# Kernel tuning notes

Measured on AMD Instinct MI355X. Metric: run time of the kernel, lower is better.

Reference implementation:

```python
import jax, jax.numpy as jnp
import numpy as np
import math

H = 16
D_MODEL = 1024
D_K = D_MODEL // H


def setup_inputs() -> dict:
    key = jax.random.key(0)
    ks = jax.random.split(key, 12)
    B, S = 4, 2048
    inp = {
        "query": jax.random.normal(ks[0], (B, S, D_MODEL), jnp.float32),
        "key": jax.random.normal(ks[1], (B, S, D_MODEL), jnp.float32),
        "value": jax.random.normal(ks[2], (B, S, D_MODEL), jnp.float32),
        # causal mask, broadcastable over heads: [B, 1, S, S]
        "mask": jnp.broadcast_to(jnp.tril(jnp.ones((S, S), bool)), (B, 1, S, S)),
    }
    sc = 1.0 / math.sqrt(D_MODEL)
    inp["Wq"] = jax.random.normal(ks[3], (D_MODEL, D_MODEL), jnp.float32) * sc
    inp["bq"] = jnp.zeros((D_MODEL,), jnp.float32)
    inp["Wk"] = jax.random.normal(ks[4], (D_MODEL, D_MODEL), jnp.float32) * sc
    inp["bk"] = jnp.zeros((D_MODEL,), jnp.float32)
    inp["Wv"] = jax.random.normal(ks[5], (D_MODEL, D_MODEL), jnp.float32) * sc
    inp["bv"] = jnp.zeros((D_MODEL,), jnp.float32)
    inp["Wo"] = jax.random.normal(ks[6], (D_MODEL, D_MODEL), jnp.float32) * sc
    inp["bo"] = jnp.zeros((D_MODEL,), jnp.float32)
    return inp


def reference(query, key, value, mask, Wq, bq, Wk, bk, Wv, bv, Wo, bo):
    B, S, D = query.shape
    # torch nn.Linear: y = x @ W.T + b; then view(B,-1,h,d_k).transpose(1,2)
    def proj(x, W, b):
        return (x @ W.T + b).reshape(B, -1, H, D_K).transpose(0, 2, 1, 3)  # [B,h,S,d_k]

    q = proj(query, Wq, bq)
    k = proj(key, Wk, bk)
    v = proj(value, Wv, bv)

    scores = jnp.einsum("bhqd,bhkd->bhqk", q, k) / math.sqrt(D_K)
    scores = jnp.where(mask, scores, jnp.finfo(scores.dtype).min)
    p_attn = jax.nn.softmax(scores, axis=-1)  # dropout: eval mode (identity)
    x = jnp.einsum("bhqk,bhkd->bhqd", p_attn, v)
    x = x.transpose(0, 2, 1, 3).reshape(B, -1, H * D_K)
    return x @ Wo.T + bo
```

## Files before the change

### kernel.cpp

```cpp
#include <hip/hip_runtime.h>
#include <hip/hip_bf16.h>

typedef unsigned short u16;
typedef unsigned int u32;
typedef __attribute__((ext_vector_type(8))) short short8;
typedef __attribute__((ext_vector_type(4))) short short4v;
typedef __attribute__((ext_vector_type(4))) float f32x4;
typedef __attribute__((ext_vector_type(4))) float float4_t;

#define DIM 1024
#define NH  16
#define DKK 64
#define SEQ 2048
#define NB  4
#define SM_SCALE 0.1803368801111244f

__device__ __forceinline__ u16 f2bf(float f) {
    __bf16 h = (__bf16)f;
    return __builtin_bit_cast(u16, h);
}

__device__ __forceinline__ f32x4 mfma_bf16(short8 a, short8 b, f32x4 c) {
    return __builtin_amdgcn_mfma_f32_16x16x32_bf16(a, b, c, 0, 0, 0);
}

__device__ __forceinline__ short8 pack8(float4_t a, float4_t b) {
    short8 v;
    v[0] = (short)f2bf(a[0]); v[1] = (short)f2bf(a[1]);
    v[2] = (short)f2bf(a[2]); v[3] = (short)f2bf(a[3]);
    v[4] = (short)f2bf(b[0]); v[5] = (short)f2bf(b[1]);
    v[6] = (short)f2bf(b[2]); v[7] = (short)f2bf(b[3]);
    return v;
}

typedef const __attribute__((address_space(1))) u32* gas1_t;
typedef __attribute__((address_space(3))) u32* las3_t;
__device__ __forceinline__ void g2l16(const void* g, void* l) {
    __builtin_amdgcn_global_load_lds((gas1_t)g, (las3_t)l, 16, 0, 0);
}

__device__ __forceinline__ float max16(const f32x4* s) {
    const float a = fmaxf(fmaxf(s[0][0], s[0][1]), fmaxf(s[0][2], s[0][3]));
    const float b = fmaxf(fmaxf(s[1][0], s[1][1]), fmaxf(s[1][2], s[1][3]));
    const float c = fmaxf(fmaxf(s[2][0], s[2][1]), fmaxf(s[2][2], s[2][3]));
    const float d = fmaxf(fmaxf(s[3][0], s[3][1]), fmaxf(s[3][2], s[3][3]));
    return fmaxf(fmaxf(a, b), fmaxf(c, d));
}

__global__ __launch_bounds__(256) void conv8(const float* __restrict__ src,
                                             u16* __restrict__ dst) {
    const int i = (blockIdx.x * 256 + threadIdx.x) * 8;
    const float4_t a = *(const float4_t*)(src + i);
    const float4_t b = *(const float4_t*)(src + i + 4);
    *(short8*)(dst + i) = pack8(a, b);
}

__global__ __launch_bounds__(256) void conv8w(const float* __restrict__ w0,
                                              const float* __restrict__ w1,
                                              const float* __restrict__ w2,
                                              const float* __restrict__ w3,
                                              u16* __restrict__ dst) {
    const int t = blockIdx.y;
    const float* s = t == 0 ? w0 : t == 1 ? w1 : t == 2 ? w2 : w3;
    const int i = (blockIdx.x * 256 + threadIdx.x) * 8;
    const float4_t a = *(const float4_t*)(s + i);
    const float4_t b = *(const float4_t*)(s + i + 4);
    *(short8*)(dst + (size_t)t * DIM * DIM + i) = pack8(a, b);
}

template<int MODE>
__global__ __launch_bounds__(256)
void gemmb(const u16* __restrict__ A, const u16* __restrict__ Bw,
           const float* __restrict__ bias, float scale,
           u16* __restrict__ Cbf, float* __restrict__ Cf)
{
    __shared__ __align__(16) u16 As[128][64];
    __shared__ __align__(16) u16 Bs[128][64];
    const int tid  = threadIdx.x;
    const int lane = tid & 63;
    const int w    = tid >> 6;
    const int wr   = w >> 1, wc = w & 1;
    const int m0   = blockIdx.y * 128;
    const int n0   = blockIdx.x * 128;
    const int lm   = lane & 15, lg = lane >> 4;
    const int srow   = lane >> 3;
    const int schunk = (lane & 7) ^ srow;

    f32x4 acc[4][4];
#pragma unroll
    for (int i = 0; i < 4; ++i)
#pragma unroll
        for (int j = 0; j < 4; ++j) acc[i][j] = (f32x4){0.f, 0.f, 0.f, 0.f};

    for (int k0 = 0; k0 < DIM; k0 += 64) {
        __syncthreads();
#pragma unroll
        for (int i = 0; i < 4; ++i) {
            g2l16(A  + (size_t)(m0 + w * 32 + i * 8 + srow) * DIM + k0 + schunk * 8,
                  &As[w * 32 + i * 8][0]);
            g2l16(Bw + (size_t)(n0 + w * 32 + i * 8 + srow) * DIM + k0 + schunk * 8,
                  &Bs[w * 32 + i * 8][0]);
        }
        __syncthreads();

        short8 af[2][4], bfr[2][4];
#pragma unroll
        for (int t = 0; t < 4; ++t)
#pragma unroll
            for (int kh = 0; kh < 2; ++kh) {
                const int c = (kh * 4 + lg) ^ (lm & 7);
                af[kh][t]  = *(const short8*)&As[wr * 64 + t * 16 + lm][c * 8];
                bfr[kh][t] = *(const short8*)&Bs[wc * 64 + t * 16 + lm][c * 8];
            }
#pragma unroll
        for (int mt = 0; mt < 4; ++mt)
#pragma unroll
            for (int nt = 0; nt < 4; ++nt) {
                acc[mt][nt] = mfma_bf16(af[0][mt], bfr[0][nt], acc[mt][nt]);
                acc[mt][nt] = mfma_bf16(af[1][mt], bfr[1][nt], acc[mt][nt]);
            }
    }

#pragma unroll
    for (int mt = 0; mt < 4; ++mt)
#pragma unroll
        for (int nt = 0; nt < 4; ++nt)
#pragma unroll
            for (int r = 0; r < 4; ++r) {
                const int m = m0 + wr * 64 + mt * 16 + lg * 4 + r;
                const int n = n0 + wc * 64 + nt * 16 + lm;
                if (MODE == 0) {
                    const float val = (acc[mt][nt][r] + bias[n]) * scale;
                    const int b = m >> 11, s = m & 2047;
                    const int h = n >> 6,  dk = n & 63;
                    Cbf[(((size_t)b * NH + h) * SEQ + s) * DKK + dk] = f2bf(val);
                } else if (MODE == 1) {
                    Cf[(size_t)m * DIM + n] = acc[mt][nt][r] + bias[n];
                } else {
                    const float val = acc[mt][nt][r] + bias[m];
                    const int h = m >> 6, dk = m & 63;
                    const int b = n >> 11, s = n & 2047;
                    Cbf[(((size_t)b * NH + h) * DKK + dk) * SEQ + s] = f2bf(val);
                }
            }
}

__global__ __launch_bounds__(256, 2)
void attn3(const u16* __restrict__ Q, const u16* __restrict__ K,
           const u16* __restrict__ Vt, u16* __restrict__ O)
{
    __shared__ __align__(16) u16 Ks[64][72];
    __shared__ __align__(16) u16 Vs[64][72];
    __shared__ __align__(16) u16 Ps[4][32][72];

    const int tid  = threadIdx.x;
    const int lane = tid & 63;
    const int w    = tid >> 6;
    const int lm   = lane & 15, lg = lane >> 4;
    const int Lr   = blockIdx.y * gridDim.x + blockIdx.x;
    const int work = (Lr & 7) * 128 + (Lr >> 3);
    const int pb   = work & 15;
    const int bh   = work >> 4;
    const int Abase = pb * 64;
    const int Bbase = SEQ - 64 - Abase;
    const int qA = Abase + 16 * w;
    const int qB = Bbase + 16 * w;
    const u16* Qp = Q  + (size_t)bh * SEQ * DKK;
    const u16* Kp = K  + (size_t)bh * SEQ * DKK;
    const u16* Vp = Vt + (size_t)bh * DKK * SEQ;

    short8 qa[2][2];
#pragma unroll
    for (int kh = 0; kh < 2; ++kh) {
        qa[0][kh] = *(const short8*)(Qp + (size_t)(qA + lm) * DKK + kh * 32 + lg * 8);
        qa[1][kh] = *(const short8*)(Qp + (size_t)(qB + lm) * DKK + kh * 32 + lg * 8);
    }

    float m_q[2] = {-INFINITY, -INFINITY};
    float l_q[2] = {0.f, 0.f};
    f32x4 o[2][4];
#pragma unroll
    for (int qt = 0; qt < 2; ++qt)
#pragma unroll
        for (int dt = 0; dt < 4; ++dt) o[qt][dt] = (f32x4){0.f, 0.f, 0.f, 0.f};

    const f32x4 zero = (f32x4){0.f, 0.f, 0.f, 0.f};
    const int srow = tid >> 3;
    const int soct = (tid & 7) * 8;
    const int kv_end = Bbase + 64;

    short8 rk0 = *(const short8*)(Kp + (size_t)srow * DKK + soct);
    short8 rk1 = *(const short8*)(Kp + (size_t)(srow + 32) * DKK + soct);
    short8 rv0 = *(const short8*)(Vp + (size_t)srow * SEQ + soct);
    short8 rv1 = *(const short8*)(Vp + (size_t)(srow + 32) * SEQ + soct);

    for (int kv0 = 0; kv0 < kv_end; kv0 += 64) {
        __syncthreads();
        *(short8*)&Ks[srow][soct]      = rk0;
        *(short8*)&Ks[srow + 32][soct] = rk1;
        *(short8*)&Vs[srow][soct]      = rv0;
        *(short8*)&Vs[srow + 32][soct] = rv1;
        const int nkv = kv0 + 64;
        if (nkv < kv_end) {
            rk0 = *(const short8*)(Kp + (size_t)(nkv + srow) * DKK + soct);
            rk1 = *(const short8*)(Kp + (size_t)(nkv + srow + 32) * DKK + soct);
            rv0 = *(const short8*)(Vp + (size_t)srow * SEQ + nkv + soct);
            rv1 = *(const short8*)(Vp + (size_t)(srow + 32) * SEQ + nkv + soct);
        }
        __syncthreads();

        const bool actA = kv0 < qA + 16;
        const bool msk[2] = { kv0 + 63 > qA, kv0 + 63 > qB };
        const int  qb[2]  = { qA, qB };

        f32x4 s[2][4];
#pragma unroll
        for (int kvt = 0; kvt < 4; ++kvt) {
            const short8 kb0 = *(const short8*)&Ks[kvt * 16 + lm][lg * 8];
            const short8 kb1 = *(const short8*)&Ks[kvt * 16 + lm][32 + lg * 8];
            s[1][kvt] = mfma_bf16(kb1, qa[1][1], mfma_bf16(kb0, qa[1][0], zero));
            if (actA)
                s[0][kvt] = mfma_bf16(kb1, qa[0][1], mfma_bf16(kb0, qa[0][0], zero));
        }

        float mx[2] = {-INFINITY, -INFINITY};
#pragma unroll
        for (int qt = 0; qt < 2; ++qt) {
            if (!qt && !actA) continue;
            if (msk[qt]) {
                const int q = qb[qt] + lm;
#pragma unroll
                for (int kvt = 0; kvt < 4; ++kvt)
#pragma unroll
                    for (int r = 0; r < 4; ++r) {
                        const int kv = kv0 + kvt * 16 + lg * 4 + r;
                        if (kv > q) s[qt][kvt][r] = -INFINITY;
                    }
            }
            float vmax = max16(s[qt]);
            vmax = fmaxf(vmax, __shfl_xor(vmax, 16));
            vmax = fmaxf(vmax, __shfl_xor(vmax, 32));
            mx[qt] = vmax;
        }

        const bool small = (!actA || mx[0] <= m_q[0] + 8.f) && (mx[1] <= m_q[1] + 8.f);
        if (__all(small)) {
#pragma unroll
            for (int qt = 0; qt < 2; ++qt) {
                if (!qt && !actA) continue;
                float part[4];
#pragma unroll
                for (int kvt = 0; kvt < 4; ++kvt) {
                    short4v pk;
                    f32x4 p;
#pragma unroll
                    for (int r = 0; r < 4; ++r) {
                        p[r] = __builtin_exp2f(s[qt][kvt][r] - m_q[qt]);
                        pk[r] = (short)f2bf(p[r]);
                    }
                    part[kvt] = (p[0] + p[1]) + (p[2] + p[3]);
                    *(short4v*)&Ps[w][qt * 16 + lm][kvt * 16 + lg * 4] = pk;
                }
                l_q[qt] += (part[0] + part[1]) + (part[2] + part[3]);
            }
        } else {
#pragma unroll
            for (int qt = 0; qt < 2; ++qt) {
                if (!qt && !actA) continue;
                const float mnew = fmaxf(m_q[qt], mx[qt]);
                const float alpha = __builtin_exp2f(m_q[qt] - mnew);
                m_q[qt] = mnew;
                float part[4];
#pragma unroll
                for (int kvt = 0; kvt < 4; ++kvt) {
                    short4v pk;
                    f32x4 p;
#pragma unroll
                    for (int r = 0; r < 4; ++r) {
                        p[r] = __builtin_exp2f(s[qt][kvt][r] - mnew);
                        pk[r] = (short)f2bf(p[r]);
                    }
                    part[kvt] = (p[0] + p[1]) + (p[2] + p[3]);
                    *(short4v*)&Ps[w][qt * 16 + lm][kvt * 16 + lg * 4] = pk;
                }
                l_q[qt] = l_q[qt] * alpha + (part[0] + part[1]) + (part[2] + part[3]);
#pragma unroll
                for (int r = 0; r < 4; ++r) {
                    const float ar = __shfl(alpha, lg * 4 + r);
#pragma unroll
                    for (int dt = 0; dt < 4; ++dt) o[qt][dt][r] *= ar;
                }
            }
        }
        asm volatile("s_waitcnt lgkmcnt(0)" ::: "memory");

        short8 pa[2][2], vbt[4][2];
#pragma unroll
        for (int qt = 0; qt < 2; ++qt)
            if (qt || actA) {
                pa[qt][0] = *(const short8*)&Ps[w][qt * 16 + lm][lg * 8];
                pa[qt][1] = *(const short8*)&Ps[w][qt * 16 + lm][32 + lg * 8];
            }
#pragma unroll
        for (int dt = 0; dt < 4; ++dt) {
            vbt[dt][0] = *(const short8*)&Vs[dt * 16 + lm][lg * 8];
            vbt[dt][1] = *(const short8*)&Vs[dt * 16 + lm][32 + lg * 8];
        }
#pragma unroll
        for (int dt = 0; dt < 4; ++dt)
#pragma unroll
            for (int qt = 0; qt < 2; ++qt) {
                if (!qt && !actA) continue;
                o[qt][dt] = mfma_bf16(pa[qt][1], vbt[dt][1],
                                      mfma_bf16(pa[qt][0], vbt[dt][0], o[qt][dt]));
            }
    }

    const int b = bh >> 4, h = bh & 15;
#pragma unroll
    for (int qt = 0; qt < 2; ++qt) {
        float lf = l_q[qt];
        lf += __shfl_xor(lf, 16);
        lf += __shfl_xor(lf, 32);
        const int qbase = qt ? qB : qA;
#pragma unroll
        for (int r = 0; r < 4; ++r) {
            const float li = 1.f / __shfl(lf, lg * 4 + r);
            const int srw = qbase + lg * 4 + r;
#pragma unroll
            for (int dt = 0; dt < 4; ++dt)
                O[(((size_t)b * SEQ + srw) * NH + h) * DKK + dt * 16 + lm] =
                    f2bf(o[qt][dt][r] * li);
        }
    }
}

extern "C" void kernel_launch(void* const* d_in, const int* in_sizes, int n_in,
                              void* d_out, int out_size, void* d_ws, size_t ws_size,
                              hipStream_t stream)
{
    const float* query = (const float*)d_in[0];
    const float* key   = (const float*)d_in[1];
    const float* value = (const float*)d_in[2];
    const float* Wq = (const float*)d_in[4];
    const float* bq = (const float*)d_in[5];
    const float* Wk = (const float*)d_in[6];
    const float* bk = (const float*)d_in[7];
    const float* Wv = (const float*)d_in[8];
    const float* bv = (const float*)d_in[9];
    const float* Wo = (const float*)d_in[10];
    const float* bo = (const float*)d_in[11];
    float* out = (float*)d_out;

    const size_t HD = (size_t)NB * NH * SEQ * DKK;
    const size_t WSZ = (size_t)DIM * DIM;
    u16* qws  = (u16*)d_ws;
    u16* kws  = qws + HD;
    u16* vtws = kws + HD;
    u16* ows  = vtws + HD;
    u16* wbf  = ows + HD;
    u16* cvt  = ows;

    dim3 gg(DIM / 128, (NB * SEQ) / 128);
    dim3 gv((NB * SEQ) / 128, DIM / 128);
    const int ca = (int)(HD / 2048);
    conv8w<<<dim3(WSZ / 2048, 4), 256, 0, stream>>>(Wq, Wk, Wv, Wo, wbf);

    conv8<<<ca, 256, 0, stream>>>(query, cvt);
    gemmb<0><<<gg, 256, 0, stream>>>(cvt, wbf, bq, SM_SCALE, qws, nullptr);
    conv8<<<ca, 256, 0, stream>>>(key, cvt);
    gemmb<0><<<gg, 256, 0, stream>>>(cvt, wbf + WSZ, bk, 1.f, kws, nullptr);
    conv8<<<ca, 256, 0, stream>>>(value, cvt);
    gemmb<2><<<gv, 256, 0, stream>>>(wbf + 2 * WSZ, cvt, bv, 1.f, vtws, nullptr);

    attn3<<<dim3(16, NB * NH), 256, 0, stream>>>(qws, kws, vtws, ows);
    gemmb<1><<<gg, 256, 0, stream>>>(ows, wbf + 3 * WSZ, bo, 1.f, nullptr, out);
}
```

Before: 235.7 us.

## Enlarge attention blocks to 512 threads with 32-row query tiles per wave

The attention kernel now runs 8 waves per block, each owning 32 contiguous query rows. Four waves cover a low query block and four cover the mirrored high block, so causal work stays balanced. Each K/V tile loaded into shared memory is shared by twice as many query rows, cutting global K/V traffic and staging loads per thread. In exchange the grid has half as many blocks, waves whose rows are fully masked sit idle at the barriers, and the larger shared P buffer and register use may limit occupancy.

```diff
diff --git a/kernel.cpp b/kernel.cpp
--- a/kernel.cpp
+++ b/kernel.cpp
@@ -145,36 +145,36 @@
             }
 }
 
-__global__ __launch_bounds__(256, 2)
-void attn3(const u16* __restrict__ Q, const u16* __restrict__ K,
+__global__ __launch_bounds__(512)
+void attn5(const u16* __restrict__ Q, const u16* __restrict__ K,
            const u16* __restrict__ Vt, u16* __restrict__ O)
 {
     __shared__ __align__(16) u16 Ks[64][72];
     __shared__ __align__(16) u16 Vs[64][72];
-    __shared__ __align__(16) u16 Ps[4][32][72];
+    __shared__ __align__(16) u16 Ps[8][32][72];
 
     const int tid  = threadIdx.x;
     const int lane = tid & 63;
     const int w    = tid >> 6;
     const int lm   = lane & 15, lg = lane >> 4;
     const int Lr   = blockIdx.y * gridDim.x + blockIdx.x;
-    const int work = (Lr & 7) * 128 + (Lr >> 3);
-    const int pb   = work & 15;
-    const int bh   = work >> 4;
-    const int Abase = pb * 64;
-    const int Bbase = SEQ - 64 - Abase;
-    const int qA = Abase + 16 * w;
-    const int qB = Bbase + 16 * w;
+    const int work = (Lr & 7) * 64 + (Lr >> 3);
+    const int pb   = work & 7;
+    const int bh   = work >> 3;
+    const int Abase = 128 * pb;
+    const int Bbase = 1920 - 128 * pb;
+    const int wv   = w & 3;
+    const int qW   = (w < 4) ? (Abase + 32 * wv) : (Bbase + 32 * wv);
     const u16* Qp = Q  + (size_t)bh * SEQ * DKK;
     const u16* Kp = K  + (size_t)bh * SEQ * DKK;
     const u16* Vp = Vt + (size_t)bh * DKK * SEQ;
 
     short8 qa[2][2];
 #pragma unroll
-    for (int kh = 0; kh < 2; ++kh) {
-        qa[0][kh] = *(const short8*)(Qp + (size_t)(qA + lm) * DKK + kh * 32 + lg * 8);
-        qa[1][kh] = *(const short8*)(Qp + (size_t)(qB + lm) * DKK + kh * 32 + lg * 8);
-    }
+    for (int qt = 0; qt < 2; ++qt)
+#pragma unroll
+        for (int kh = 0; kh < 2; ++kh)
+            qa[qt][kh] = *(const short8*)(Qp + (size_t)(qW + qt * 16 + lm) * DKK + kh * 32 + lg * 8);
 
     float m_q[2] = {-INFINITY, -INFINITY};
     float l_q[2] = {0.f, 0.f};
@@ -187,133 +187,129 @@
     const f32x4 zero = (f32x4){0.f, 0.f, 0.f, 0.f};
     const int srow = tid >> 3;
     const int soct = (tid & 7) * 8;
-    const int kv_end = Bbase + 64;
-
-    short8 rk0 = *(const short8*)(Kp + (size_t)srow * DKK + soct);
-    short8 rk1 = *(const short8*)(Kp + (size_t)(srow + 32) * DKK + soct);
-    short8 rv0 = *(const short8*)(Vp + (size_t)srow * SEQ + soct);
-    short8 rv1 = *(const short8*)(Vp + (size_t)(srow + 32) * SEQ + soct);
+    const int kv_end = Bbase + 128;
+
+    short8 rk = *(const short8*)(Kp + (size_t)srow * DKK + soct);
+    short8 rv = *(const short8*)(Vp + (size_t)srow * SEQ + soct);
 
     for (int kv0 = 0; kv0 < kv_end; kv0 += 64) {
         __syncthreads();
-        *(short8*)&Ks[srow][soct]      = rk0;
-        *(short8*)&Ks[srow + 32][soct] = rk1;
-        *(short8*)&Vs[srow][soct]      = rv0;
-        *(short8*)&Vs[srow + 32][soct] = rv1;
+        *(short8*)&Ks[srow][soct] = rk;
+        *(short8*)&Vs[srow][soct] = rv;
         const int nkv = kv0 + 64;
         if (nkv < kv_end) {
-            rk0 = *(const short8*)(Kp + (size_t)(nkv + srow) * DKK + soct);
-            rk1 = *(const short8*)(Kp + (size_t)(nkv + srow + 32) * DKK + soct);
-            rv0 = *(const short8*)(Vp + (size_t)srow * SEQ + nkv + soct);
-            rv1 = *(const short8*)(Vp + (size_t)(srow + 32) * SEQ + nkv + soct);
+            rk = *(const short8*)(Kp + (size_t)(nkv + srow) * DKK + soct);
+            rv = *(const short8*)(Vp + (size_t)srow * SEQ + nkv + soct);
         }
         __syncthreads();
 
-        const bool actA = kv0 < qA + 16;
-        const bool msk[2] = { kv0 + 63 > qA, kv0 + 63 > qB };
-        const int  qb[2]  = { qA, qB };
-
-        f32x4 s[2][4];
-#pragma unroll
-        for (int kvt = 0; kvt < 4; ++kvt) {
-            const short8 kb0 = *(const short8*)&Ks[kvt * 16 + lm][lg * 8];
-            const short8 kb1 = *(const short8*)&Ks[kvt * 16 + lm][32 + lg * 8];
-            s[1][kvt] = mfma_bf16(kb1, qa[1][1], mfma_bf16(kb0, qa[1][0], zero));
-            if (actA)
-                s[0][kvt] = mfma_bf16(kb1, qa[0][1], mfma_bf16(kb0, qa[0][0], zero));
+        const bool act[2] = { kv0 < qW + 16, kv0 < qW + 32 };
+        if (act[1]) {
+            const bool msk[2] = { kv0 + 63 > qW, kv0 + 63 > qW + 16 };
+
+            f32x4 s[2][4];
+#pragma unroll
+            for (int kvt = 0; kvt < 4; ++kvt) {
+                const short8 kb0 = *(const short8*)&Ks[kvt * 16 + lm][lg * 8];
+                const short8 kb1 = *(const short8*)&Ks[kvt * 16 + lm][32 + lg * 8];
+                s[1][kvt] = mfma_bf16(kb1, qa[1][1], mfma_bf16(kb0, qa[1][0], zero));
+                if (act[0])
+                    s[0][kvt] = mfma_bf16(kb1, qa[0][1], mfma_bf16(kb0, qa[0][0], zero));
+            }
+
+            float mx[2] = {-INFINITY, -INFINITY};
+#pragma unroll
+            for (int qt = 0; qt < 2; ++qt) {
+                if (!act[qt]) continue;
+                if (msk[qt]) {
+                    const int q = qW + qt * 16 + lm;
+#pragma unroll
+                    for (int kvt = 0; kvt < 4; ++kvt)
+#pragma unroll
+                        for (int r = 0; r < 4; ++r) {
+                            const int kv = kv0 + kvt * 16 + lg * 4 + r;
+                            if (kv > q) s[qt][kvt][r] = -INFINITY;
+                        }
+                }
+                float vmax = max16(s[qt]);
+                vmax = fmaxf(vmax, __shfl_xor(vmax, 16));
+                vmax = fmaxf(vmax, __shfl_xor(vmax, 32));
+                mx[qt] = vmax;
+            }
+
+            const bool small = (!act[0] || mx[0] <= m_q[0] + 8.f) &&
+                               (mx[1] <= m_q[1] + 8.f);
+            if (__all(small)) {
+#pragma unroll
+                for (int qt = 0; qt < 2; ++qt) {
+                    if (!act[qt]) continue;
+                    float part[4];
+#pragma unroll
+                    for (int kvt = 0; kvt < 4; ++kvt) {
+                        short4v pk;
+                        f32x4 p;
+#pragma unroll
+                        for (int r = 0; r < 4; ++r) {
+                            p[r] = __builtin_exp2f(s[qt][kvt][r] - m_q[qt]);
+                            pk[r] = (short)f2bf(p[r]);
+                        }
+                        part[kvt] = (p[0] + p[1]) + (p[2] + p[3]);
+                        *(short4v*)&Ps[w][qt * 16 + lm][kvt * 16 + lg * 4] = pk;
+                    }
+                    l_q[qt] += (part[0] + part[1]) + (part[2] + part[3]);
+                }
+            } else {
+#pragma unroll
+                for (int qt = 0; qt < 2; ++qt) {
+                    if (!act[qt]) continue;
+                    const float mnew = fmaxf(m_q[qt], mx[qt]);
+                    const float alpha = __builtin_exp2f(m_q[qt] - mnew);
+                    m_q[qt] = mnew;
+                    float part[4];
+#pragma unroll
+                    for (int kvt = 0; kvt < 4; ++kvt) {
+                        short4v pk;
+                        f32x4 p;
+#pragma unroll
+                        for (int r = 0; r < 4; ++r) {
+                            p[r] = __builtin_exp2f(s[qt][kvt][r] - mnew);
+                            pk[r] = (short)f2bf(p[r]);
+                        }
+                        part[kvt] = (p[0] + p[1]) + (p[2] + p[3]);
+                        *(short4v*)&Ps[w][qt * 16 + lm][kvt * 16 + lg * 4] = pk;
+                    }
+                    l_q[qt] = l_q[qt] * alpha + (part[0] + part[1]) + (part[2] + part[3]);
+#pragma unroll
+                    for (int r = 0; r < 4; ++r) {
+                        const float ar = __shfl(alpha, lg * 4 + r);
+#pragma unroll
+                        for (int dt = 0; dt < 4; ++dt) o[qt][dt][r] *= ar;
+                    }
+                }
+            }
+            asm volatile("s_waitcnt lgkmcnt(0)" ::: "memory");
+
+            short8 pa[2][2], vbt[4][2];
+#pragma unroll
+            for (int qt = 0; qt < 2; ++qt)
+                if (act[qt]) {
+                    pa[qt][0] = *(const short8*)&Ps[w][qt * 16 + lm][lg * 8];
+                    pa[qt][1] = *(const short8*)&Ps[w][qt * 16 + lm][32 + lg * 8];
+                }
+#pragma unroll
+            for (int dt = 0; dt < 4; ++dt) {
+                vbt[dt][0] = *(const short8*)&Vs[dt * 16 + lm][lg * 8];
+                vbt[dt][1] = *(const short8*)&Vs[dt * 16 + lm][32 + lg * 8];
+            }
+#pragma unroll
+            for (int dt = 0; dt < 4; ++dt)
+#pragma unroll
+                for (int qt = 0; qt < 2; ++qt) {
+                    if (!act[qt]) continue;
+                    o[qt][dt] = mfma_bf16(pa[qt][1], vbt[dt][1],
+                                          mfma_bf16(pa[qt][0], vbt[dt][0], o[qt][dt]));
+                }
         }
-
-        float mx[2] = {-INFINITY, -INFINITY};
-#pragma unroll
-        for (int qt = 0; qt < 2; ++qt) {
-            if (!qt && !actA) continue;
-            if (msk[qt]) {
-                const int q = qb[qt] + lm;
-#pragma unroll
-                for (int kvt = 0; kvt < 4; ++kvt)
-#pragma unroll
-                    for (int r = 0; r < 4; ++r) {
-                        const int kv = kv0 + kvt * 16 + lg * 4 + r;
-                        if (kv > q) s[qt][kvt][r] = -INFINITY;
-                    }
-            }
-            float vmax = max16(s[qt]);
-            vmax = fmaxf(vmax, __shfl_xor(vmax, 16));
-            vmax = fmaxf(vmax, __shfl_xor(vmax, 32));
-            mx[qt] = vmax;
-        }
-
-        const bool small = (!actA || mx[0] <= m_q[0] + 8.f) && (mx[1] <= m_q[1] + 8.f);
-        if (__all(small)) {
-#pragma unroll
-            for (int qt = 0; qt < 2; ++qt) {
-                if (!qt && !actA) continue;
-                float part[4];
-#pragma unroll
-                for (int kvt = 0; kvt < 4; ++kvt) {
-                    short4v pk;
-                    f32x4 p;
-#pragma unroll
-                    for (int r = 0; r < 4; ++r) {
-                        p[r] = __builtin_exp2f(s[qt][kvt][r] - m_q[qt]);
-                        pk[r] = (short)f2bf(p[r]);
-                    }
-                    part[kvt] = (p[0] + p[1]) + (p[2] + p[3]);
-                    *(short4v*)&Ps[w][qt * 16 + lm][kvt * 16 + lg * 4] = pk;
-                }
-                l_q[qt] += (part[0] + part[1]) + (part[2] + part[3]);
-            }
-        } else {
-#pragma unroll
-            for (int qt = 0; qt < 2; ++qt) {
-                if (!qt && !actA) continue;
-                const float mnew = fmaxf(m_q[qt], mx[qt]);
-                const float alpha = __builtin_exp2f(m_q[qt] - mnew);
-                m_q[qt] = mnew;
-                float part[4];
-#pragma unroll
-                for (int kvt = 0; kvt < 4; ++kvt) {
-                    short4v pk;
-                    f32x4 p;
-#pragma unroll
-                    for (int r = 0; r < 4; ++r) {
-                        p[r] = __builtin_exp2f(s[qt][kvt][r] - mnew);
-                        pk[r] = (short)f2bf(p[r]);
-                    }
-                    part[kvt] = (p[0] + p[1]) + (p[2] + p[3]);
-                    *(short4v*)&Ps[w][qt * 16 + lm][kvt * 16 + lg * 4] = pk;
-                }
-                l_q[qt] = l_q[qt] * alpha + (part[0] + part[1]) + (part[2] + part[3]);
-#pragma unroll
-                for (int r = 0; r < 4; ++r) {
-                    const float ar = __shfl(alpha, lg * 4 + r);
-#pragma unroll
-                    for (int dt = 0; dt < 4; ++dt) o[qt][dt][r] *= ar;
-                }
-            }
-        }
-        asm volatile("s_waitcnt lgkmcnt(0)" ::: "memory");
-
-        short8 pa[2][2], vbt[4][2];
-#pragma unroll
-        for (int qt = 0; qt < 2; ++qt)
-            if (qt || actA) {
-                pa[qt][0] = *(const short8*)&Ps[w][qt * 16 + lm][lg * 8];
-                pa[qt][1] = *(const short8*)&Ps[w][qt * 16 + lm][32 + lg * 8];
-            }
-#pragma unroll
-        for (int dt = 0; dt < 4; ++dt) {
-            vbt[dt][0] = *(const short8*)&Vs[dt * 16 + lm][lg * 8];
-            vbt[dt][1] = *(const short8*)&Vs[dt * 16 + lm][32 + lg * 8];
-        }
-#pragma unroll
-        for (int dt = 0; dt < 4; ++dt)
-#pragma unroll
-            for (int qt = 0; qt < 2; ++qt) {
-                if (!qt && !actA) continue;
-                o[qt][dt] = mfma_bf16(pa[qt][1], vbt[dt][1],
-                                      mfma_bf16(pa[qt][0], vbt[dt][0], o[qt][dt]));
-            }
     }
 
     const int b = bh >> 4, h = bh & 15;
@@ -322,11 +318,10 @@
         float lf = l_q[qt];
         lf += __shfl_xor(lf, 16);
         lf += __shfl_xor(lf, 32);
-        const int qbase = qt ? qB : qA;
 #pragma unroll
         for (int r = 0; r < 4; ++r) {
             const float li = 1.f / __shfl(lf, lg * 4 + r);
-            const int srw = qbase + lg * 4 + r;
+            const int srw = qW + qt * 16 + lg * 4 + r;
 #pragma unroll
             for (int dt = 0; dt < 4; ++dt)
                 O[(((size_t)b * SEQ + srw) * NH + h) * DKK + dt * 16 + lm] =
@@ -373,6 +368,6 @@
     conv8<<<ca, 256, 0, stream>>>(value, cvt);
     gemmb<2><<<gv, 256, 0, stream>>>(wbf + 2 * WSZ, cvt, bv, 1.f, vtws, nullptr);
 
-    attn3<<<dim3(16, NB * NH), 256, 0, stream>>>(qws, kws, vtws, ows);
+    attn5<<<dim3(8, 64), 512, 0, stream>>>(qws, kws, vtws, ows);
     gemmb<1><<<gg, 256, 0, stream>>>(ows, wbf + 3 * WSZ, bo, 1.f, nullptr, out);
 }
```

Result: no change. 239.4 us (+1.6%).

## Fuse fp32-to-bf16 activation conversion into projection GEMMs and batch Q/K launches

Applied to the files above, without the earlier changes.

Removes the three standalone conv8 passes. The Q, K and V projection GEMMs now load fp32 activations directly, convert them to bf16 in registers and store them to swizzled LDS. Q and K projections are merged into one launch using blockIdx.z to pick input, weight, bias, scale and output. This avoids writing and re-reading bf16 activation copies, but activation staging now goes through registers with synchronous global loads instead of async global-to-LDS loads, and each A tile is re-read as fp32 by every column block, which doubles those load bytes.

```diff
diff --git a/kernel.cpp b/kernel.cpp
--- a/kernel.cpp
+++ b/kernel.cpp
@@ -13,6 +13,8 @@
 #define DKK 64
 #define SEQ 2048
 #define NB  4
+#define HDSZ ((size_t)NB * NH * SEQ * DKK)
+#define WSZ  ((size_t)DIM * DIM)
 #define SM_SCALE 0.1803368801111244f
 
 __device__ __forceinline__ u16 f2bf(float f) {
@@ -47,12 +49,17 @@
     return fmaxf(fmaxf(a, b), fmaxf(c, d));
 }
 
-__global__ __launch_bounds__(256) void conv8(const float* __restrict__ src,
-                                             u16* __restrict__ dst) {
-    const int i = (blockIdx.x * 256 + threadIdx.x) * 8;
-    const float4_t a = *(const float4_t*)(src + i);
-    const float4_t b = *(const float4_t*)(src + i + 4);
-    *(short8*)(dst + i) = pack8(a, b);
+__device__ __forceinline__ void stage_f32(const float* __restrict__ src,
+                                          u16 (*dst)[64], int tid, int k0) {
+#pragma unroll
+    for (int p = 0; p < 4; ++p) {
+        const int r = p * 32 + (tid >> 3);
+        const int c = tid & 7;
+        const float* s = src + (size_t)r * DIM + k0 + c * 8;
+        const float4_t a = *(const float4_t*)s;
+        const float4_t b = *(const float4_t*)(s + 4);
+        *(short8*)&dst[r][(c ^ (r & 7)) * 8] = pack8(a, b);
+    }
 }
 
 __global__ __launch_bounds__(256) void conv8w(const float* __restrict__ w0,
@@ -65,14 +72,15 @@
     const int i = (blockIdx.x * 256 + threadIdx.x) * 8;
     const float4_t a = *(const float4_t*)(s + i);
     const float4_t b = *(const float4_t*)(s + i + 4);
-    *(short8*)(dst + (size_t)t * DIM * DIM + i) = pack8(a, b);
+    *(short8*)(dst + (size_t)t * WSZ + i) = pack8(a, b);
 }
 
 template<int MODE>
 __global__ __launch_bounds__(256)
-void gemmb(const u16* __restrict__ A, const u16* __restrict__ Bw,
-           const float* __restrict__ bias, float scale,
-           u16* __restrict__ Cbf, float* __restrict__ Cf)
+void gemmb(const float* __restrict__ F0, const float* __restrict__ F1,
+           const u16* __restrict__ Hb, const u16* __restrict__ Wb,
+           const float* __restrict__ bias0, const float* __restrict__ bias1,
+           u16* __restrict__ Cb, float* __restrict__ Cf)
 {
     __shared__ __align__(16) u16 As[128][64];
     __shared__ __align__(16) u16 Bs[128][64];
@@ -82,10 +90,14 @@
     const int wr   = w >> 1, wc = w & 1;
     const int m0   = blockIdx.y * 128;
     const int n0   = blockIdx.x * 128;
+    const int z    = (MODE == 0) ? blockIdx.z : 0;
     const int lm   = lane & 15, lg = lane >> 4;
     const int srow   = lane >> 3;
     const int schunk = (lane & 7) ^ srow;
 
+    const float* Act = (MODE == 0) ? (z ? F1 : F0) : F0;
+    const u16*   Wz  = (MODE == 0) ? Wb + (size_t)z * WSZ : Wb;
+
     f32x4 acc[4][4];
 #pragma unroll
     for (int i = 0; i < 4; ++i)
@@ -94,12 +106,26 @@
 
     for (int k0 = 0; k0 < DIM; k0 += 64) {
         __syncthreads();
-#pragma unroll
-        for (int i = 0; i < 4; ++i) {
-            g2l16(A  + (size_t)(m0 + w * 32 + i * 8 + srow) * DIM + k0 + schunk * 8,
-                  &As[w * 32 + i * 8][0]);
-            g2l16(Bw + (size_t)(n0 + w * 32 + i * 8 + srow) * DIM + k0 + schunk * 8,
-                  &Bs[w * 32 + i * 8][0]);
+        if (MODE == 0) {
+#pragma unroll
+            for (int i = 0; i < 4; ++i)
+                g2l16(Wz + (size_t)(n0 + w * 32 + i * 8 + srow) * DIM + k0 + schunk * 8,
+                      &Bs[w * 32 + i * 8][0]);
+            stage_f32(Act + (size_t)m0 * DIM, As, tid, k0);
+        } else if (MODE == 1) {
+#pragma unroll
+            for (int i = 0; i < 4; ++i) {
+                g2l16(Hb + (size_t)(m0 + w * 32 + i * 8 + srow) * DIM + k0 + schunk * 8,
+                      &As[w * 32 + i * 8][0]);
+                g2l16(Wz + (size_t)(n0 + w * 32 + i * 8 + srow) * DIM + k0 + schunk * 8,
+                      &Bs[w * 32 + i * 8][0]);
+            }
+        } else {
+#pragma unroll
+            for (int i = 0; i < 4; ++i)
+                g2l16(Hb + (size_t)(m0 + w * 32 + i * 8 + srow) * DIM + k0 + schunk * 8,
+                      &As[w * 32 + i * 8][0]);
+            stage_f32(Act + (size_t)n0 * DIM, Bs, tid, k0);
         }
         __syncthreads();
 
@@ -120,6 +146,10 @@
                 acc[mt][nt] = mfma_bf16(af[1][mt], bfr[1][nt], acc[mt][nt]);
             }
     }
+
+    const float scale = (MODE == 0 && z == 0) ? SM_SCALE : 1.f;
+    const float* bias = (MODE == 0 && z) ? bias1 : bias0;
+    u16* Cz = (MODE == 0) ? Cb + (size_t)z * HDSZ : Cb;
 
 #pragma unroll
     for (int mt = 0; mt < 4; ++mt)
@@ -133,14 +163,14 @@
                     const float val = (acc[mt][nt][r] + bias[n]) * scale;
                     const int b = m >> 11, s = m & 2047;
                     const int h = n >> 6,  dk = n & 63;
-                    Cbf[(((size_t)b * NH + h) * SEQ + s) * DKK + dk] = f2bf(val);
+                    Cz[(((size_t)b * NH + h) * SEQ + s) * DKK + dk] = f2bf(val);
                 } else if (MODE == 1) {
                     Cf[(size_t)m * DIM + n] = acc[mt][nt][r] + bias[n];
                 } else {
                     const float val = acc[mt][nt][r] + bias[m];
                     const int h = m >> 6, dk = m & 63;
                     const int b = n >> 11, s = n & 2047;
-                    Cbf[(((size_t)b * NH + h) * DKK + dk) * SEQ + s] = f2bf(val);
+                    Cz[(((size_t)b * NH + h) * DKK + dk) * SEQ + s] = f2bf(val);
                 }
             }
 }
@@ -352,27 +382,22 @@
     const float* bo = (const float*)d_in[11];
     float* out = (float*)d_out;
 
-    const size_t HD = (size_t)NB * NH * SEQ * DKK;
-    const size_t WSZ = (size_t)DIM * DIM;
     u16* qws  = (u16*)d_ws;
-    u16* kws  = qws + HD;
-    u16* vtws = kws + HD;
-    u16* ows  = vtws + HD;
-    u16* wbf  = ows + HD;
-    u16* cvt  = ows;
-
+    u16* kws  = qws + HDSZ;
+    u16* vtws = kws + HDSZ;
+    u16* ows  = vtws + HDSZ;
+    u16* wbf  = ows + HDSZ;
+
+    dim3 gqk(DIM / 128, (NB * SEQ) / 128, 2);
+    dim3 gv((NB * SEQ) / 128, DIM / 128);
     dim3 gg(DIM / 128, (NB * SEQ) / 128);
-    dim3 gv((NB * SEQ) / 128, DIM / 128);
-    const int ca = (int)(HD / 2048);
+
     conv8w<<<dim3(WSZ / 2048, 4), 256, 0, stream>>>(Wq, Wk, Wv, Wo, wbf);
-
-    conv8<<<ca, 256, 0, stream>>>(query, cvt);
-    gemmb<0><<<gg, 256, 0, stream>>>(cvt, wbf, bq, SM_SCALE, qws, nullptr);
-    conv8<<<ca, 256, 0, stream>>>(key, cvt);
-    gemmb<0><<<gg, 256, 0, stream>>>(cvt, wbf + WSZ, bk, 1.f, kws, nullptr);
-    conv8<<<ca, 256, 0, stream>>>(value, cvt);
-    gemmb<2><<<gv, 256, 0, stream>>>(wbf + 2 * WSZ, cvt, bv, 1.f, vtws, nullptr);
-
+    gemmb<0><<<gqk, 256, 0, stream>>>(query, key, nullptr, wbf, bq, bk,
+                                      qws, nullptr);
+    gemmb<2><<<gv, 256, 0, stream>>>(value, nullptr, wbf + 2 * WSZ, nullptr,
+                                     bv, nullptr, vtws, nullptr);
     attn3<<<dim3(16, NB * NH), 256, 0, stream>>>(qws, kws, vtws, ows);
-    gemmb<1><<<gg, 256, 0, stream>>>(ows, wbf + 3 * WSZ, bo, 1.f, nullptr, out);
-}
+    gemmb<1><<<gg, 256, 0, stream>>>(nullptr, nullptr, ows, wbf + 3 * WSZ,
+                                     bo, nullptr, nullptr, out);
+}
```

Measured after the change: 251.9 us. 6.9% more time.
